# Performance work log

Hardware: AMD Instinct MI355X
Metric: run time of the kernel (lower is better)

Reference implementation:

```python
import jax, jax.numpy as jnp
import numpy as np

NEG_SLOPE = 0.2
MASK_FILL = -9e10


def setup_inputs() -> dict:
    key = jax.random.key(0)
    ks = jax.random.split(key, 8)
    B, N, D = 8, 2048, 64
    return {
        "opes_mask_adj": jax.random.randint(ks[0], (B, N, N), 0, 2, dtype=jnp.int32),
        "opes_mask_job": jax.random.randint(ks[1], (B, N, N), 0, 2, dtype=jnp.int32),
        "batch_idxes": jnp.arange(B, dtype=jnp.int64),
        "feats": jax.random.normal(ks[2], (B, N, D), dtype=jnp.float32),
        "W_ope": jax.random.normal(ks[3], (D, D), dtype=jnp.float32) * (1.0 / np.sqrt(D)),
        "attn_src": jax.random.normal(ks[4], (D,), dtype=jnp.float32) * (1.0 / np.sqrt(D)),
        "attn_dst": jax.random.normal(ks[5], (D,), dtype=jnp.float32) * (1.0 / np.sqrt(D)),
        "lambda_params": jax.random.normal(ks[6], (D, 2), dtype=jnp.float32),
    }


def reference(opes_mask_adj, opes_mask_job, batch_idxes, feats, W_ope, attn_src, attn_dst, lambda_params):
    # h_ope: [B, N, D]  (Linear with weight [out,in]: x @ W^T)
    h_ope = jnp.einsum("bnd,od->bno", feats, W_ope)
    a_src = h_ope @ attn_src  # [B, N]
    a_dst = h_ope @ attn_dst  # [B, N]
    e = a_src[:, :, None] + a_dst[:, None, :]  # [B, N, N]
    e = jnp.where(e >= 0, e, NEG_SLOPE * e)  # leaky relu

    mask_adj = opes_mask_adj[batch_idxes] == 1
    alpha_adj = jax.nn.softmax(jnp.where(mask_adj, e, MASK_FILL), axis=-1)
    h_adj = jnp.einsum("bnm,bmd->bnd", alpha_adj, h_ope)

    mask_job = opes_mask_job[batch_idxes] == 1
    alpha_job = jax.nn.softmax(jnp.where(mask_job, e, MASK_FILL), axis=-1)
    h_job = jnp.einsum("bnm,bmd->bnd", alpha_job, h_ope)

    # in_dim == out_dim -> identity residual (res_fc is None)
    lambdas = jax.nn.softmax(lambda_params, axis=1)  # [D, 2]
    lambda_adj, lambda_job = lambdas[:, 0], lambdas[:, 1]
    return lambda_adj * h_adj + lambda_job * h_job + feats
```

## Files before the change

### kernel.cpp

```cpp
#include <hip/hip_runtime.h>

#define B_ 8
#define N_ 2048
#define D_ 64

typedef __attribute__((ext_vector_type(8))) short bf16x8;
typedef __attribute__((ext_vector_type(4))) float f32x4;
typedef __attribute__((ext_vector_type(4))) int i32x4;

__device__ inline unsigned short f32_bf16_rne(float f) {
    unsigned u = __float_as_uint(f);
    u += 0x7fffu + ((u >> 16) & 1u);
    return (unsigned short)(u >> 16);
}

__device__ inline unsigned cvt_pk_bf16(float lo, float hi) {
    unsigned r;
    asm("v_cvt_pk_bf16_f32 %0, %1, %2" : "=v"(r) : "v"(lo), "v"(hi));
    return r;
}

__global__ __launch_bounds__(256) void prep_kernel(
    const float* __restrict__ feats, const float* __restrict__ W,
    const float* __restrict__ attn_src, const float* __restrict__ attn_dst,
    unsigned short* __restrict__ hT, float* __restrict__ a_src,
    float* __restrict__ F1, float* __restrict__ F2) {
    __shared__ float w_lds[64 * 65];
    __shared__ float f_lds[32 * 64];
    __shared__ unsigned short hT_lds[64 * 40];

    const int t = threadIdx.x;
    const int b = blockIdx.x >> 6;
    const int rowbase = (blockIdx.x & 63) * 32;

#pragma unroll
    for (int k = 0; k < 4; k++) {
        int lin = (k * 256 + t) * 4;
        float4 v = *(const float4*)(W + lin);
        int o = lin >> 6, d = lin & 63;
        float* p = &w_lds[o * 65 + d];
        p[0] = v.x; p[1] = v.y; p[2] = v.z; p[3] = v.w;
    }
#pragma unroll
    for (int k = 0; k < 2; k++) {
        int lin = (k * 256 + t) * 4;
        float4 v = *(const float4*)(feats + (size_t)(b * N_ + rowbase) * D_ + lin);
        float* p = &f_lds[lin];
        p[0] = v.x; p[1] = v.y; p[2] = v.z; p[3] = v.w;
    }
    __syncthreads();

    const int w = t >> 6;
    const int o = t & 63;
    float acc[8] = {0.f, 0.f, 0.f, 0.f, 0.f, 0.f, 0.f, 0.f};
#pragma unroll 8
    for (int d = 0; d < 64; d++) {
        float wv = w_lds[o * 65 + d];
#pragma unroll
        for (int rr = 0; rr < 8; rr++)
            acc[rr] = fmaf(f_lds[(w * 8 + rr) * 64 + d], wv, acc[rr]);
    }
    float as_ = attn_src[o], ad_ = attn_dst[o];
#pragma unroll
    for (int rr = 0; rr < 8; rr++) {
        int row = rowbase + w * 8 + rr;
        float s1 = acc[rr] * as_;
        float s2 = acc[rr] * ad_;
#pragma unroll
        for (int off = 32; off; off >>= 1) {
            s1 += __shfl_xor(s1, off);
            s2 += __shfl_xor(s2, off);
        }
        if (o == 0) {
            a_src[b * N_ + row] = s1;
            F1[b * N_ + row] = __expf(s2);
            F2[b * N_ + row] = __expf(0.2f * s2);
        }
        hT_lds[o * 40 + w * 8 + rr] = f32_bf16_rne(acc[rr]);
    }
    __syncthreads();
    const int d = t >> 2, seg = t & 3;
    uint4 vv = *(const uint4*)(&hT_lds[d * 40 + seg * 8]);
    *(uint4*)(hT + ((size_t)(b * 64 + d) * N_ + rowbase + seg * 8)) = vv;
}

__global__ __launch_bounds__(256, 3) void attn_kernel(
    const int* __restrict__ mask_adj, const int* __restrict__ mask_job,
    const int* __restrict__ batch_idxes,
    const unsigned short* __restrict__ hT, const float* __restrict__ a_src,
    const float* __restrict__ F1, const float* __restrict__ F2,
    const float* __restrict__ feats, const float* __restrict__ lambda_params,
    float* __restrict__ out) {
    __shared__ f32x4 redbuf[3][10][64];

    const int t = threadIdx.x;
    const int b = blockIdx.x >> 7;
    const int rowbase = (blockIdx.x & 127) * 16;
    const int wid = t >> 6, lane = t & 63;
    const int m = lane & 15, q = lane >> 4;
    const int i_a = rowbase + m;

    int bi = batch_idxes[b];
    bi = (bi < 0) ? 0 : ((bi >= B_) ? (B_ - 1) : bi);

    const int jb = wid * 512 + q * 8;
    const int* mA = mask_adj + ((size_t)bi * N_ + i_a) * N_ + jb;
    const int* mJ = mask_job + ((size_t)bi * N_ + i_a) * N_ + jb;
    const float* f1p = F1 + b * N_ + jb;
    const float* f2p = F2 + b * N_ + jb;
    const unsigned short* hp0 = hT + (size_t)b * 64 * N_ + (size_t)m * N_ + jb;
    const unsigned short* hp1 = hp0 + 16 * N_;
    const unsigned short* hp2 = hp0 + 32 * N_;
    const unsigned short* hp3 = hp0 + 48 * N_;

    const float s = a_src[b * N_ + i_a];
    const float cmpT = __expf(-s);
    const float cT = __expf(-0.8f * s);

    f32x4 accA[4], accJ[4], accZA, accZJ;
    const f32x4 z4 = {0.f, 0.f, 0.f, 0.f};
#pragma unroll
    for (int dd = 0; dd < 4; dd++) { accA[dd] = z4; accJ[dd] = z4; }
    accZA = z4; accZJ = z4;
    bf16x8 ones;
#pragma unroll
    for (int i = 0; i < 8; i++) ones[i] = (short)0x3F80;

#pragma unroll
    for (int st = 0; st < 16; st++) {
        const int off = st * 32;
        i32x4 a0 = __builtin_nontemporal_load((const i32x4*)(mA + off));
        i32x4 a1 = __builtin_nontemporal_load((const i32x4*)(mA + off + 4));
        i32x4 b0 = __builtin_nontemporal_load((const i32x4*)(mJ + off));
        i32x4 b1 = __builtin_nontemporal_load((const i32x4*)(mJ + off + 4));
        float4 g0 = *(const float4*)(f1p + off);
        float4 g1 = *(const float4*)(f1p + off + 4);
        float4 h0 = *(const float4*)(f2p + off);
        float4 h1 = *(const float4*)(f2p + off + 4);
        bf16x8 fb0 = *(const bf16x8*)(hp0 + off);
        bf16x8 fb1 = *(const bf16x8*)(hp1 + off);
        bf16x8 fb2 = *(const bf16x8*)(hp2 + off);
        bf16x8 fb3 = *(const bf16x8*)(hp3 + off);

        int ma[8] = {a0[0], a0[1], a0[2], a0[3], a1[0], a1[1], a1[2], a1[3]};
        int mj[8] = {b0[0], b0[1], b0[2], b0[3], b1[0], b1[1], b1[2], b1[3]};
        float f1v[8] = {g0.x, g0.y, g0.z, g0.w, g1.x, g1.y, g1.z, g1.w};
        float f2v[8] = {h0.x, h0.y, h0.z, h0.w, h1.x, h1.y, h1.z, h1.w};

        unsigned ua[4], uj[4];
#pragma unroll
        for (int wp = 0; wp < 4; wp++) {
            float p0 = (f1v[2 * wp] >= cmpT) ? f1v[2 * wp] : cT * f2v[2 * wp];
            float p1 = (f1v[2 * wp + 1] >= cmpT) ? f1v[2 * wp + 1] : cT * f2v[2 * wp + 1];
            float pa0 = (ma[2 * wp] == 1) ? p0 : 0.f;
            float pa1 = (ma[2 * wp + 1] == 1) ? p1 : 0.f;
            float pj0 = (mj[2 * wp] == 1) ? p0 : 0.f;
            float pj1 = (mj[2 * wp + 1] == 1) ? p1 : 0.f;
            ua[wp] = cvt_pk_bf16(pa0, pa1);
            uj[wp] = cvt_pk_bf16(pj0, pj1);
        }
        union { uint4 u; bf16x8 v; } fa_, fj_;
        fa_.u = make_uint4(ua[0], ua[1], ua[2], ua[3]);
        fj_.u = make_uint4(uj[0], uj[1], uj[2], uj[3]);
        bf16x8 fa = fa_.v, fj = fj_.v;

        accZA = __builtin_amdgcn_mfma_f32_16x16x32_bf16(fa, ones, accZA, 0, 0, 0);
        accZJ = __builtin_amdgcn_mfma_f32_16x16x32_bf16(fj, ones, accZJ, 0, 0, 0);
        accA[0] = __builtin_amdgcn_mfma_f32_16x16x32_bf16(fa, fb0, accA[0], 0, 0, 0);
        accJ[0] = __builtin_amdgcn_mfma_f32_16x16x32_bf16(fj, fb0, accJ[0], 0, 0, 0);
        accA[1] = __builtin_amdgcn_mfma_f32_16x16x32_bf16(fa, fb1, accA[1], 0, 0, 0);
        accJ[1] = __builtin_amdgcn_mfma_f32_16x16x32_bf16(fj, fb1, accJ[1], 0, 0, 0);
        accA[2] = __builtin_amdgcn_mfma_f32_16x16x32_bf16(fa, fb2, accA[2], 0, 0, 0);
        accJ[2] = __builtin_amdgcn_mfma_f32_16x16x32_bf16(fj, fb2, accJ[2], 0, 0, 0);
        accA[3] = __builtin_amdgcn_mfma_f32_16x16x32_bf16(fa, fb3, accA[3], 0, 0, 0);
        accJ[3] = __builtin_amdgcn_mfma_f32_16x16x32_bf16(fj, fb3, accJ[3], 0, 0, 0);
    }

    if (wid) {
#pragma unroll
        for (int c = 0; c < 4; c++) {
            redbuf[wid - 1][c][lane] = accA[c];
            redbuf[wid - 1][4 + c][lane] = accJ[c];
        }
        redbuf[wid - 1][8][lane] = accZA;
        redbuf[wid - 1][9][lane] = accZJ;
    }
    __syncthreads();
    if (wid == 0) {
#pragma unroll
        for (int wv = 0; wv < 3; wv++) {
#pragma unroll
            for (int c = 0; c < 4; c++) {
                accA[c] += redbuf[wv][c][lane];
                accJ[c] += redbuf[wv][4 + c][lane];
            }
            accZA += redbuf[wv][8][lane];
            accZJ += redbuf[wv][9][lane];
        }
        float invA[4], invJ[4];
#pragma unroll
        for (int r = 0; r < 4; r++) {
            invA[r] = 1.f / accZA[r];
            invJ[r] = 1.f / accZJ[r];
        }
#pragma unroll
        for (int dd = 0; dd < 4; dd++) {
            int d = dd * 16 + m;
            float l0 = lambda_params[d * 2];
            float l1 = lambda_params[d * 2 + 1];
            float e0 = __expf(l0), e1 = __expf(l1);
            float inv = 1.f / (e0 + e1);
            float la = e0 * inv, lj = e1 * inv;
#pragma unroll
            for (int r = 0; r < 4; r++) {
                int i = rowbase + q * 4 + r;
                size_t off = (size_t)(b * N_ + i) * D_ + d;
                out[off] = la * accA[dd][r] * invA[r] + lj * accJ[dd][r] * invJ[r] + feats[off];
            }
        }
    }
}

extern "C" void kernel_launch(void* const* d_in, const int* in_sizes, int n_in,
                              void* d_out, int out_size, void* d_ws, size_t ws_size,
                              hipStream_t stream) {
    const int* mask_adj = (const int*)d_in[0];
    const int* mask_job = (const int*)d_in[1];
    const int* batch_idxes = (const int*)d_in[2];
    const float* feats = (const float*)d_in[3];
    const float* W = (const float*)d_in[4];
    const float* attn_src = (const float*)d_in[5];
    const float* attn_dst = (const float*)d_in[6];
    const float* lambda_params = (const float*)d_in[7];
    float* out = (float*)d_out;

    unsigned short* hT = (unsigned short*)d_ws;
    float* a_src = (float*)((char*)d_ws + (size_t)B_ * 64 * N_ * 2);
    float* F1 = a_src + B_ * N_;
    float* F2 = F1 + B_ * N_;

    prep_kernel<<<B_ * (N_ / 32), 256, 0, stream>>>(feats, W, attn_src, attn_dst,
                                                    hT, a_src, F1, F2);
    attn_kernel<<<B_ * (N_ / 16), 256, 0, stream>>>(mask_adj, mask_job, batch_idxes,
                                                    hT, a_src, F1, F2, feats,
                                                    lambda_params, out);
}
```

Measured before the change: 319.5 us.

## Split attention key range across two blocks and add final combine kernel

After: 492.5 us. 54.2% more time.

```diff
diff --git a/kernel.cpp b/kernel.cpp
--- a/kernel.cpp
+++ b/kernel.cpp
@@ -3,6 +3,7 @@
 #define B_ 8
 #define N_ 2048
 #define D_ 64
+#define PSTRIDE 2080
 
 typedef __attribute__((ext_vector_type(8))) short bf16x8;
 typedef __attribute__((ext_vector_type(4))) float f32x4;
@@ -84,18 +85,19 @@
     *(uint4*)(hT + ((size_t)(b * 64 + d) * N_ + rowbase + seg * 8)) = vv;
 }
 
-__global__ __launch_bounds__(256, 3) void attn_kernel(
+__global__ __launch_bounds__(256, 8) void attn_kernel(
     const int* __restrict__ mask_adj, const int* __restrict__ mask_job,
     const int* __restrict__ batch_idxes,
     const unsigned short* __restrict__ hT, const float* __restrict__ a_src,
     const float* __restrict__ F1, const float* __restrict__ F2,
-    const float* __restrict__ feats, const float* __restrict__ lambda_params,
-    float* __restrict__ out) {
-    __shared__ f32x4 redbuf[3][10][64];
+    float* __restrict__ part) {
+    __shared__ f32x4 redbuf[3][5][64];
 
     const int t = threadIdx.x;
-    const int b = blockIdx.x >> 7;
-    const int rowbase = (blockIdx.x & 127) * 16;
+    const int half = blockIdx.x & 1;
+    const int rowtile = (blockIdx.x >> 1) & 127;
+    const int b = blockIdx.x >> 8;
+    const int rowbase = rowtile * 16;
     const int wid = t >> 6, lane = t & 63;
     const int m = lane & 15, q = lane >> 4;
     const int i_a = rowbase + m;
@@ -103,7 +105,7 @@
     int bi = batch_idxes[b];
     bi = (bi < 0) ? 0 : ((bi >= B_) ? (B_ - 1) : bi);
 
-    const int jb = wid * 512 + q * 8;
+    const int jb = half * 1024 + wid * 256 + q * 8;
     const int* mA = mask_adj + ((size_t)bi * N_ + i_a) * N_ + jb;
     const int* mJ = mask_job + ((size_t)bi * N_ + i_a) * N_ + jb;
     const float* f1p = F1 + b * N_ + jb;
@@ -127,7 +129,7 @@
     for (int i = 0; i < 8; i++) ones[i] = (short)0x3F80;
 
 #pragma unroll
-    for (int st = 0; st < 16; st++) {
+    for (int st = 0; st < 8; st++) {
         const int off = st * 32;
         i32x4 a0 = __builtin_nontemporal_load((const i32x4*)(mA + off));
         i32x4 a1 = __builtin_nontemporal_load((const i32x4*)(mA + off + 4));
@@ -178,47 +180,74 @@
 
     if (wid) {
 #pragma unroll
-        for (int c = 0; c < 4; c++) {
-            redbuf[wid - 1][c][lane] = accA[c];
-            redbuf[wid - 1][4 + c][lane] = accJ[c];
-        }
-        redbuf[wid - 1][8][lane] = accZA;
-        redbuf[wid - 1][9][lane] = accZJ;
+        for (int c = 0; c < 4; c++) redbuf[wid - 1][c][lane] = accA[c];
+        redbuf[wid - 1][4][lane] = accZA;
     }
     __syncthreads();
     if (wid == 0) {
 #pragma unroll
         for (int wv = 0; wv < 3; wv++) {
 #pragma unroll
-            for (int c = 0; c < 4; c++) {
-                accA[c] += redbuf[wv][c][lane];
-                accJ[c] += redbuf[wv][4 + c][lane];
+            for (int c = 0; c < 4; c++) accA[c] += redbuf[wv][c][lane];
+            accZA += redbuf[wv][4][lane];
+        }
+    }
+    __syncthreads();
+    if (wid) {
+#pragma unroll
+        for (int c = 0; c < 4; c++) redbuf[wid - 1][c][lane] = accJ[c];
+        redbuf[wid - 1][4][lane] = accZJ;
+    }
+    __syncthreads();
+    if (wid == 0) {
+#pragma unroll
+        for (int wv = 0; wv < 3; wv++) {
+#pragma unroll
+            for (int c = 0; c < 4; c++) accJ[c] += redbuf[wv][c][lane];
+            accZJ += redbuf[wv][4][lane];
+        }
+        float* pp = part + (size_t)blockIdx.x * PSTRIDE;
+#pragma unroll
+        for (int dd = 0; dd < 4; dd++) {
+#pragma unroll
+            for (int r = 0; r < 4; r++) {
+                int idx = (q * 4 + r) * 64 + dd * 16 + m;
+                pp[idx] = accA[dd][r];
+                pp[1024 + idx] = accJ[dd][r];
             }
-            accZA += redbuf[wv][8][lane];
-            accZJ += redbuf[wv][9][lane];
-        }
-        float invA[4], invJ[4];
-#pragma unroll
-        for (int r = 0; r < 4; r++) {
-            invA[r] = 1.f / accZA[r];
-            invJ[r] = 1.f / accZJ[r];
-        }
-#pragma unroll
-        for (int dd = 0; dd < 4; dd++) {
-            int d = dd * 16 + m;
-            float l0 = lambda_params[d * 2];
-            float l1 = lambda_params[d * 2 + 1];
-            float e0 = __expf(l0), e1 = __expf(l1);
-            float inv = 1.f / (e0 + e1);
-            float la = e0 * inv, lj = e1 * inv;
+        }
+        if (m == 0) {
 #pragma unroll
             for (int r = 0; r < 4; r++) {
-                int i = rowbase + q * 4 + r;
-                size_t off = (size_t)(b * N_ + i) * D_ + d;
-                out[off] = la * accA[dd][r] * invA[r] + lj * accJ[dd][r] * invJ[r] + feats[off];
+                pp[2048 + q * 4 + r] = accZA[r];
+                pp[2064 + q * 4 + r] = accZJ[r];
             }
         }
     }
+}
+
+__global__ __launch_bounds__(256) void final_kernel(
+    const float* __restrict__ part, const float* __restrict__ feats,
+    const float* __restrict__ lambda_params, float* __restrict__ out) {
+    const int e = blockIdx.x * 256 + threadIdx.x;
+    const int d = e & 63;
+    const int i = (e >> 6) & (N_ - 1);
+    const int b = e >> 17;
+    const int rowtile = i >> 4, ii = i & 15;
+
+    const float* p0 = part + (size_t)(((b * 128 + rowtile) * 2) + 0) * PSTRIDE;
+    const float* p1 = p0 + PSTRIDE;
+
+    float A = p0[ii * 64 + d] + p1[ii * 64 + d];
+    float J = p0[1024 + ii * 64 + d] + p1[1024 + ii * 64 + d];
+    float ZA = p0[2048 + ii] + p1[2048 + ii];
+    float ZJ = p0[2064 + ii] + p1[2064 + ii];
+
+    float l0 = lambda_params[d * 2];
+    float l1 = lambda_params[d * 2 + 1];
+    float e0 = __expf(l0), e1 = __expf(l1);
+    float inv = 1.f / (e0 + e1);
+    out[e] = (e0 * inv) * A / ZA + (e1 * inv) * J / ZJ + feats[e];
 }
 
 extern "C" void kernel_launch(void* const* d_in, const int* in_sizes, int n_in,
@@ -234,14 +263,15 @@
     const float* lambda_params = (const float*)d_in[7];
     float* out = (float*)d_out;
 
-    unsigned short* hT = (unsigned short*)d_ws;
-    float* a_src = (float*)((char*)d_ws + (size_t)B_ * 64 * N_ * 2);
+    float* part = (float*)d_ws;
+    unsigned short* hT = (unsigned short*)((char*)d_ws + (size_t)2048 * PSTRIDE * 4);
+    float* a_src = (float*)((char*)hT + (size_t)B_ * 64 * N_ * 2);
     float* F1 = a_src + B_ * N_;
     float* F2 = F1 + B_ * N_;
 
     prep_kernel<<<B_ * (N_ / 32), 256, 0, stream>>>(feats, W, attn_src, attn_dst,
                                                     hT, a_src, F1, F2);
-    attn_kernel<<<B_ * (N_ / 16), 256, 0, stream>>>(mask_adj, mask_job, batch_idxes,
-                                                    hT, a_src, F1, F2, feats,
-                                                    lambda_params, out);
-}
+    attn_kernel<<<B_ * (N_ / 16) * 2, 256, 0, stream>>>(mask_adj, mask_job, batch_idxes,
+                                                        hT, a_src, F1, F2, part);
+    final_kernel<<<B_ * N_ * D_ / 256, 256, 0, stream>>>(part, feats, lambda_params, out);
+}
```
